# Optimization experiments

Hardware: AMD Instinct MI355X
Metric: run time of the kernel (lower is better)

Reference implementation:

```python
import jax, jax.numpy as jnp
import numpy as np

N, E, DIN, H = 100000, 1600000, 128, 128


def gcn_conv(x, W, b, row, col, ew, n):
    """PyG GCNConv with add_self_loops=True, symmetric normalization.

    deg[i] = sum of edge weights into i (col) + 1 (self loop weight).
    norm_e = deg^{-1/2}[row_e] * ew_e * deg^{-1/2}[col_e]
    out[col] += norm_e * (x @ W)[row]; self-loop contributes deg^{-1}[i] * xw[i].
    """
    xw = x @ W  # [n, H]
    deg = jax.ops.segment_sum(ew, col, num_segments=n) + 1.0  # self-loop weight 1
    dinv = jax.lax.rsqrt(deg)  # deg >= 1 so safe
    norm = dinv[row] * ew * dinv[col]  # [E]
    agg = jax.ops.segment_sum(norm[:, None] * xw[row], col, num_segments=n)
    agg = agg + (dinv * dinv)[:, None] * xw  # self loops
    return agg + b


def setup_inputs() -> dict:
    key = jax.random.key(0)
    ks = jax.random.split(key, 9)
    x = jax.random.normal(ks[0], (N, DIN), jnp.float32)
    edge_index = jax.random.randint(ks[1], (2, E), 0, N, dtype=jnp.int64)
    edge_attr = jax.random.uniform(ks[2], (E,), jnp.float32)
    s_in = 1.0 / np.sqrt(DIN)
    s_h = 1.0 / np.sqrt(H)
    W1 = jax.random.normal(ks[3], (DIN, H), jnp.float32) * s_in
    b1 = jnp.zeros((H,), jnp.float32)
    W2 = jax.random.normal(ks[4], (H, H), jnp.float32) * s_h
    b2 = jnp.zeros((H,), jnp.float32)
    W3 = jax.random.normal(ks[5], (H, H), jnp.float32) * s_h
    b3 = jnp.zeros((H,), jnp.float32)
    return {"x": x, "edge_index": edge_index, "edge_attr": edge_attr,
            "W1": W1, "b1": b1, "W2": W2, "b2": b2, "W3": W3, "b3": b3}


def reference(x, edge_index, edge_attr, W1, b1, W2, b2, W3, b3):
    row, col = edge_index[0], edge_index[1]
    n = x.shape[0]
    h = jax.nn.relu(gcn_conv(x, W1, b1, row, col, edge_attr, n))
    h = jax.nn.relu(gcn_conv(h, W2, b2, row, col, edge_attr, n))
    h = jax.nn.relu(gcn_conv(h, W3, b3, row, col, edge_attr, n))
    return h
```

## Files before the change

### kernel.cpp

```cpp
#include <hip/hip_runtime.h>
#include <hip/hip_fp16.h>

#define CAP 64
#define BSH 7
#define BCAP 2560
#define NBMAX 1024

typedef _Float16 half8 __attribute__((ext_vector_type(8)));
typedef float f32x4 __attribute__((ext_vector_type(4)));


__global__ __launch_bounds__(256) void k_init(int* gcur, int nbkt) {
    int i = blockIdx.x * 256 + threadIdx.x;
    if (i < nbkt) gcur[i] = 0;
}

__global__ __launch_bounds__(256) void k_bucket(const int* __restrict__ row,
                                                const int* __restrict__ col,
                                                const float* __restrict__ ew,
                                                int* gcur, int2* sortedE,
                                                int e, int nbkt) {
    __shared__ int lcnt[NBMAX];
    __shared__ int lbase[NBMAX];
    int tid = threadIdx.x;
    for (int b = tid; b < nbkt; b += 256) lcnt[b] = 0;
    __syncthreads();
    int base = blockIdx.x * 2048;
    int bk[8], rk[8], rx[8], rwi[8];
#pragma unroll
    for (int u = 0; u < 8; ++u) {
        int i = base + tid + u * 256;
        bk[u] = -1;
        if (i < e) {
            int c = col[i];
            bk[u] = c >> BSH;
            rx[u] = row[i] | ((c & ((1 << BSH) - 1)) << 17);
            rwi[u] = __float_as_int(ew[i]);
            rk[u] = atomicAdd(&lcnt[bk[u]], 1);
        }
    }
    __syncthreads();
    for (int b = tid; b < nbkt; b += 256) {
        int c = lcnt[b];
        lbase[b] = c ? atomicAdd(&gcur[b], c) : 0;
    }
    __syncthreads();
#pragma unroll
    for (int u = 0; u < 8; ++u) {
        if (bk[u] >= 0) {
            int pos = lbase[bk[u]] + rk[u];
            if (pos < BCAP) sortedE[(long)bk[u] * BCAP + pos] = make_int2(rx[u], rwi[u]);
        }
    }
}

__global__ __launch_bounds__(256) void k_csr(const int2* __restrict__ sortedE,
                                             const int* __restrict__ gcur,
                                             int2* __restrict__ csr,
                                             int* __restrict__ counts,
                                             float* __restrict__ dinv, int n) {
    int bkt = blockIdx.x;
    __shared__ int c128[128];
    __shared__ float s128[128];
    int tid = threadIdx.x;
    if (tid < 128) { c128[tid] = 0; s128[tid] = 0.f; }
    __syncthreads();
    int cnt = gcur[bkt];
    if (cnt > BCAP) cnt = BCAP;
    for (int j = tid; j < cnt; j += 256) {
        int2 rec = sortedE[(long)bkt * BCAP + j];
        int cl = rec.x >> 17;
        int r0 = rec.x & 0x1FFFF;
        float w = __int_as_float(rec.y);
        int r = atomicAdd(&c128[cl], 1);
        if (r < CAP) csr[((long)((bkt << BSH) + cl)) * CAP + r] = make_int2(r0, rec.y);
        atomicAdd(&s128[cl], w);
    }
    __syncthreads();
    if (tid < 128) {
        int node = (bkt << BSH) + tid;
        if (node < n) {
            int c = c128[tid];
            counts[node] = c < CAP ? c : CAP;
            dinv[node] = rsqrtf(s128[tid] + 1.0f);
        }
    }
}

__global__ __launch_bounds__(256) void k_norm(const int* __restrict__ counts,
                                              const float* __restrict__ dinv,
                                              int2* csr, int n) {
    int gw = (blockIdx.x * 256 + threadIdx.x) >> 6;
    int lane = threadIdx.x & 63;
    if (gw >= n) return;
    int cnt = __builtin_amdgcn_readfirstlane(counts[gw]);
    float dc = dinv[gw];
    if (lane < cnt) {
        long idx = (long)gw * CAP + lane;
        int2 ent = csr[idx];
        float w = dinv[ent.x] * __int_as_float(ent.y) * dc;
        csr[idx] = make_int2(ent.x, __float_as_int(w));
    }
}

__global__ __launch_bounds__(256) void k_wt(const float* __restrict__ W1,
                                            const float* __restrict__ W2,
                                            const float* __restrict__ W3,
                                            __half* __restrict__ Wt) {
    int m = blockIdx.x >> 6;
    int kb = (blockIdx.x & 63) << 1;
    const float* W = m == 0 ? W1 : (m == 1 ? W2 : W3);
    __half* T = Wt + (long)m * 16384;
    int k = kb + (threadIdx.x >> 7);
    int nn = threadIdx.x & 127;
    T[nn * 128 + k] = __float2half(W[k * 128 + nn]);
}


__global__ __launch_bounds__(256) void k_gemm(const float* __restrict__ Xf,
                                              const __half* __restrict__ Xh,
                                              const __half* __restrict__ Wt,
                                              __half* __restrict__ Yh, int n) {
    __shared__ __half Wl[128 * 128];
    int tid = threadIdx.x;
    {
        const uint4* src = (const uint4*)Wt;
#pragma unroll
        for (int i = 0; i < 8; ++i) {
            int c = tid + 256 * i;
            int nrow = c >> 4, k8 = c & 15;
            uint4 v = src[c];
            int byte = nrow * 256 + ((k8 * 16) ^ ((nrow & 7) << 4));
            *(uint4*)((char*)Wl + byte) = v;
        }
    }
    __syncthreads();
    int wid = tid >> 6, lane = tid & 63;
    int l16 = lane & 15, lq = lane >> 4;
    long row0 = (long)blockIdx.x * 128 + wid * 32;
    f32x4 acc[2][8] = {};
#pragma unroll
    for (int ks = 0; ks < 4; ++ks) {
        int k0 = ks * 32;
        half8 a[2];
#pragma unroll
        for (int mt = 0; mt < 2; ++mt) {
            long r = row0 + mt * 16 + l16;
            if (r >= n) r = n - 1;
            if (Xf) {
                const float* px = Xf + r * 128 + k0 + lq * 8;
                float4 f0 = *(const float4*)px;
                float4 f1 = *(const float4*)(px + 4);
                half8 h;
                h[0] = (_Float16)f0.x; h[1] = (_Float16)f0.y;
                h[2] = (_Float16)f0.z; h[3] = (_Float16)f0.w;
                h[4] = (_Float16)f1.x; h[5] = (_Float16)f1.y;
                h[6] = (_Float16)f1.z; h[7] = (_Float16)f1.w;
                a[mt] = h;
            } else {
                a[mt] = *(const half8*)(Xh + r * 128 + k0 + lq * 8);
            }
        }
#pragma unroll
        for (int nt = 0; nt < 8; ++nt) {
            int nrow = nt * 16 + l16;
            int byte = nrow * 256 + (((k0 + lq * 8) * 2) ^ ((nrow & 7) << 4));
            half8 b = *(const half8*)((char*)Wl + byte);
            acc[0][nt] = __builtin_amdgcn_mfma_f32_16x16x32_f16(a[0], b, acc[0][nt], 0, 0, 0);
            acc[1][nt] = __builtin_amdgcn_mfma_f32_16x16x32_f16(a[1], b, acc[1][nt], 0, 0, 0);
        }
    }
#pragma unroll
    for (int mt = 0; mt < 2; ++mt) {
#pragma unroll
        for (int r = 0; r < 4; ++r) {
            long rw = row0 + mt * 16 + lq * 4 + r;
            if (rw < n) {
#pragma unroll
                for (int nt = 0; nt < 8; ++nt) {
                    Yh[rw * 128 + nt * 16 + l16] = __float2half(acc[mt][nt][r]);
                }
            }
        }
    }
}

__global__ __launch_bounds__(256) void k_agg(const int2* __restrict__ csr,
                                             const int* __restrict__ counts,
                                             const float* __restrict__ dinv,
                                             const __half* __restrict__ xwh,
                                             const float* __restrict__ bias,
                                             __half* __restrict__ outh,
                                             float* __restrict__ outf, int n) {
    int gw = (blockIdx.x * 256 + threadIdx.x) >> 6;
    int lane = threadIdx.x & 63;
    if (gw >= n) return;
    int cnt = __builtin_amdgcn_readfirstlane(counts[gw]);
    int g = lane >> 4;
    int c16 = lane & 15;
    float di = dinv[gw];
    half8 sv8 = *(const half8*)(xwh + (long)gw * 128 + c16 * 8);
    float4 bv0 = *(const float4*)(bias + c16 * 8);
    float4 bv1 = *(const float4*)(bias + c16 * 8 + 4);
    int2 ent = make_int2(gw, 0);
    if (lane < cnt) ent = csr[(long)gw * CAP + lane];
    float acc[8] = {};
    int mr = (cnt + 15) & ~15;
    for (int j = 0; j < mr; j += 16) {
        half8 hv[4];
        float wv[4];
#pragma unroll
        for (int q = 0; q < 4; ++q) {
            int r = __shfl(ent.x, j + q * 4 + g);
            hv[q] = *(const half8*)(xwh + (long)r * 128 + c16 * 8);
        }
#pragma unroll
        for (int q = 0; q < 4; ++q) wv[q] = __int_as_float(__shfl(ent.y, j + q * 4 + g));
#pragma unroll
        for (int q = 0; q < 4; ++q) {
#pragma unroll
            for (int t = 0; t < 8; ++t) acc[t] = fmaf(wv[q], (float)hv[q][t], acc[t]);
        }
    }
#pragma unroll
    for (int t = 0; t < 8; ++t) {
        acc[t] += __shfl_xor(acc[t], 16);
        acc[t] += __shfl_xor(acc[t], 32);
    }
    float d2 = di * di;
    float o[8];
    o[0] = fmaxf(acc[0] + d2 * (float)sv8[0] + bv0.x, 0.f);
    o[1] = fmaxf(acc[1] + d2 * (float)sv8[1] + bv0.y, 0.f);
    o[2] = fmaxf(acc[2] + d2 * (float)sv8[2] + bv0.z, 0.f);
    o[3] = fmaxf(acc[3] + d2 * (float)sv8[3] + bv0.w, 0.f);
    o[4] = fmaxf(acc[4] + d2 * (float)sv8[4] + bv1.x, 0.f);
    o[5] = fmaxf(acc[5] + d2 * (float)sv8[5] + bv1.y, 0.f);
    o[6] = fmaxf(acc[6] + d2 * (float)sv8[6] + bv1.z, 0.f);
    o[7] = fmaxf(acc[7] + d2 * (float)sv8[7] + bv1.w, 0.f);
    if (g == 0) {
        if (outh) {
            half8 ho;
#pragma unroll
            for (int t = 0; t < 8; ++t) ho[t] = (_Float16)o[t];
            *(half8*)(outh + (long)gw * 128 + c16 * 8) = ho;
        }
        if (outf) {
            float4 f0 = make_float4(o[0], o[1], o[2], o[3]);
            float4 f1 = make_float4(o[4], o[5], o[6], o[7]);
            *(float4*)(outf + (long)gw * 128 + c16 * 8) = f0;
            *(float4*)(outf + (long)gw * 128 + c16 * 8 + 4) = f1;
        }
    }
}


extern "C" void kernel_launch(void* const* d_in, const int* in_sizes, int n_in,
                              void* d_out, int out_size, void* d_ws, size_t ws_size,
                              hipStream_t stream) {
    const float* x  = (const float*)d_in[0];
    const int*   ei = (const int*)d_in[1];
    const float* ew = (const float*)d_in[2];
    const float* W1 = (const float*)d_in[3];
    const float* b1 = (const float*)d_in[4];
    const float* W2 = (const float*)d_in[5];
    const float* b2 = (const float*)d_in[6];
    const float* W3 = (const float*)d_in[7];
    const float* b3 = (const float*)d_in[8];

    const int n = in_sizes[0] / 128;
    const int e = in_sizes[2];
    const int* row = ei;
    const int* col = ei + e;
    const int nbkt = (n + (1 << BSH) - 1) >> BSH;

    char* p = (char*)d_ws;
    auto alloc = [&](size_t bytes) {
        char* q = p;
        p += (bytes + 255) & ~(size_t)255;
        return q;
    };
    int*    gcur    = (int*)alloc((size_t)nbkt * 4);
    int*    counts  = (int*)alloc((size_t)n * 4);
    float*  dinv    = (float*)alloc((size_t)n * 4);
    __half* Wt      = (__half*)alloc((size_t)3 * 16384 * 2);
    int2*   sortedE = (int2*)alloc((size_t)nbkt * BCAP * 8);
    int2*   csr     = (int2*)alloc((size_t)n * CAP * 8);
    __half* xwh     = (__half*)alloc((size_t)n * 128 * 2);
    __half* h       = (__half*)alloc((size_t)n * 128 * 2);
    (void)ws_size; (void)n_in; (void)out_size;

    int gb = (n + 127) / 128;
    int ab = ((size_t)n * 64 + 255) / 256;
    int sb = (e + 2047) / 2048;

    k_init  <<<(nbkt + 255) / 256, 256, 0, stream>>>(gcur, nbkt);
    k_bucket<<<sb, 256, 0, stream>>>(row, col, ew, gcur, sortedE, e, nbkt);
    k_csr   <<<nbkt, 256, 0, stream>>>(sortedE, gcur, csr, counts, dinv, n);
    k_norm  <<<ab, 256, 0, stream>>>(counts, dinv, csr, n);
    k_wt    <<<192, 256, 0, stream>>>(W1, W2, W3, Wt);

    k_gemm<<<gb, 256, 0, stream>>>(x, (const __half*)nullptr, Wt, xwh, n);
    k_agg <<<ab, 256, 0, stream>>>(csr, counts, dinv, xwh, b1, h, (float*)nullptr, n);
    k_gemm<<<gb, 256, 0, stream>>>((const float*)nullptr, h, Wt + 16384, xwh, n);
    k_agg <<<ab, 256, 0, stream>>>(csr, counts, dinv, xwh, b2, h, (float*)nullptr, n);
    k_gemm<<<gb, 256, 0, stream>>>((const float*)nullptr, h, Wt + 32768, xwh, n);
    k_agg <<<ab, 256, 0, stream>>>(csr, counts, dinv, xwh, b3, (__half*)nullptr, (float*)d_out, n);
}
```

Measured before the change: 316.5 us.

## Pack CSR entries into 32-bit ints with fp16 weights and restructure aggregation loop

Each CSR entry now packs a 17-bit source index and an fp16 edge weight into one 32-bit int, halving CSR storage and the bytes read in normalization and aggregation. The aggregation loop now processes 8 edges per step plus a 4-edge tail instead of rounding up to 16, which avoids padded gathers of the node's own row. The init kernel is replaced with a memset. Weights lose precision by being stored as fp16.

```diff
diff --git a/kernel.cpp b/kernel.cpp
--- a/kernel.cpp
+++ b/kernel.cpp
@@ -9,11 +9,13 @@
 typedef _Float16 half8 __attribute__((ext_vector_type(8)));
 typedef float f32x4 __attribute__((ext_vector_type(4)));
 
-
-__global__ __launch_bounds__(256) void k_init(int* gcur, int nbkt) {
-    int i = blockIdx.x * 256 + threadIdx.x;
-    if (i < nbkt) gcur[i] = 0;
-}
+__device__ __forceinline__ int pack_ent(int r, float w) {
+    return r | ((int)__half_as_ushort(__float2half(w)) << 17);
+}
+__device__ __forceinline__ float ent_w(int ent) {
+    return __half2float(__ushort_as_half((unsigned short)((unsigned)ent >> 17)));
+}
+
 
 __global__ __launch_bounds__(256) void k_bucket(const int* __restrict__ row,
                                                 const int* __restrict__ col,
@@ -56,7 +58,7 @@
 
 __global__ __launch_bounds__(256) void k_csr(const int2* __restrict__ sortedE,
                                              const int* __restrict__ gcur,
-                                             int2* __restrict__ csr,
+                                             int* __restrict__ pcsr,
                                              int* __restrict__ counts,
                                              float* __restrict__ dinv, int n) {
     int bkt = blockIdx.x;
@@ -73,7 +75,7 @@
         int r0 = rec.x & 0x1FFFF;
         float w = __int_as_float(rec.y);
         int r = atomicAdd(&c128[cl], 1);
-        if (r < CAP) csr[((long)((bkt << BSH) + cl)) * CAP + r] = make_int2(r0, rec.y);
+        if (r < CAP) pcsr[((long)((bkt << BSH) + cl)) * CAP + r] = pack_ent(r0, w);
         atomicAdd(&s128[cl], w);
     }
     __syncthreads();
@@ -89,7 +91,7 @@
 
 __global__ __launch_bounds__(256) void k_norm(const int* __restrict__ counts,
                                               const float* __restrict__ dinv,
-                                              int2* csr, int n) {
+                                              int* pcsr, int n) {
     int gw = (blockIdx.x * 256 + threadIdx.x) >> 6;
     int lane = threadIdx.x & 63;
     if (gw >= n) return;
@@ -97,9 +99,10 @@
     float dc = dinv[gw];
     if (lane < cnt) {
         long idx = (long)gw * CAP + lane;
-        int2 ent = csr[idx];
-        float w = dinv[ent.x] * __int_as_float(ent.y) * dc;
-        csr[idx] = make_int2(ent.x, __float_as_int(w));
+        int ent = pcsr[idx];
+        int r = ent & 0x1FFFF;
+        float w = dinv[r] * ent_w(ent) * dc;
+        pcsr[idx] = pack_ent(r, w);
     }
 }
 
@@ -185,7 +188,7 @@
     }
 }
 
-__global__ __launch_bounds__(256) void k_agg(const int2* __restrict__ csr,
+__global__ __launch_bounds__(256) void k_agg(const int* __restrict__ pcsr,
                                              const int* __restrict__ counts,
                                              const float* __restrict__ dinv,
                                              const __half* __restrict__ xwh,
@@ -202,25 +205,30 @@
     half8 sv8 = *(const half8*)(xwh + (long)gw * 128 + c16 * 8);
     float4 bv0 = *(const float4*)(bias + c16 * 8);
     float4 bv1 = *(const float4*)(bias + c16 * 8 + 4);
-    int2 ent = make_int2(gw, 0);
-    if (lane < cnt) ent = csr[(long)gw * CAP + lane];
+    int ent = gw;
+    if (lane < cnt) ent = pcsr[(long)gw * CAP + lane];
     float acc[8] = {};
-    int mr = (cnt + 15) & ~15;
-    for (int j = 0; j < mr; j += 16) {
-        half8 hv[4];
-        float wv[4];
-#pragma unroll
-        for (int q = 0; q < 4; ++q) {
-            int r = __shfl(ent.x, j + q * 4 + g);
-            hv[q] = *(const half8*)(xwh + (long)r * 128 + c16 * 8);
-        }
-#pragma unroll
-        for (int q = 0; q < 4; ++q) wv[q] = __int_as_float(__shfl(ent.y, j + q * 4 + g));
-#pragma unroll
-        for (int q = 0; q < 4; ++q) {
-#pragma unroll
-            for (int t = 0; t < 8; ++t) acc[t] = fmaf(wv[q], (float)hv[q][t], acc[t]);
-        }
+    int j = 0;
+    int mr8 = cnt & ~7;
+    for (; j < mr8; j += 8) {
+        int eA = __shfl(ent, j + g);
+        int eB = __shfl(ent, j + 4 + g);
+        long rA = eA & 0x1FFFF, rB = eB & 0x1FFFF;
+        half8 hA = *(const half8*)(xwh + rA * 128 + c16 * 8);
+        half8 hB = *(const half8*)(xwh + rB * 128 + c16 * 8);
+        float wA = ent_w(eA), wB = ent_w(eB);
+#pragma unroll
+        for (int t = 0; t < 8; ++t) acc[t] = fmaf(wA, (float)hA[t], acc[t]);
+#pragma unroll
+        for (int t = 0; t < 8; ++t) acc[t] = fmaf(wB, (float)hB[t], acc[t]);
+    }
+    for (; j < cnt; j += 4) {
+        int eA = __shfl(ent, j + g);
+        long rA = eA & 0x1FFFF;
+        half8 hA = *(const half8*)(xwh + rA * 128 + c16 * 8);
+        float wA = ent_w(eA);
+#pragma unroll
+        for (int t = 0; t < 8; ++t) acc[t] = fmaf(wA, (float)hA[t], acc[t]);
     }
 #pragma unroll
     for (int t = 0; t < 8; ++t) {
@@ -284,7 +292,7 @@
     float*  dinv    = (float*)alloc((size_t)n * 4);
     __half* Wt      = (__half*)alloc((size_t)3 * 16384 * 2);
     int2*   sortedE = (int2*)alloc((size_t)nbkt * BCAP * 8);
-    int2*   csr     = (int2*)alloc((size_t)n * CAP * 8);
+    int*    pcsr    = (int*)alloc((size_t)n * CAP * 4);
     __half* xwh     = (__half*)alloc((size_t)n * 128 * 2);
     __half* h       = (__half*)alloc((size_t)n * 128 * 2);
     (void)ws_size; (void)n_in; (void)out_size;
@@ -293,16 +301,16 @@
     int ab = ((size_t)n * 64 + 255) / 256;
     int sb = (e + 2047) / 2048;
 
-    k_init  <<<(nbkt + 255) / 256, 256, 0, stream>>>(gcur, nbkt);
+    hipMemsetAsync(gcur, 0, (size_t)nbkt * 4, stream);
     k_bucket<<<sb, 256, 0, stream>>>(row, col, ew, gcur, sortedE, e, nbkt);
-    k_csr   <<<nbkt, 256, 0, stream>>>(sortedE, gcur, csr, counts, dinv, n);
-    k_norm  <<<ab, 256, 0, stream>>>(counts, dinv, csr, n);
+    k_csr   <<<nbkt, 256, 0, stream>>>(sortedE, gcur, pcsr, counts, dinv, n);
+    k_norm  <<<ab, 256, 0, stream>>>(counts, dinv, pcsr, n);
     k_wt    <<<192, 256, 0, stream>>>(W1, W2, W3, Wt);
 
     k_gemm<<<gb, 256, 0, stream>>>(x, (const __half*)nullptr, Wt, xwh, n);
-    k_agg <<<ab, 256, 0, stream>>>(csr, counts, dinv, xwh, b1, h, (float*)nullptr, n);
+    k_agg <<<ab, 256, 0, stream>>>(pcsr, counts, dinv, xwh, b1, h, (float*)nullptr, n);
     k_gemm<<<gb, 256, 0, stream>>>((const float*)nullptr, h, Wt + 16384, xwh, n);
-    k_agg <<<ab, 256, 0, stream>>>(csr, counts, dinv, xwh, b2, h, (float*)nullptr, n);
+    k_agg <<<ab, 256, 0, stream>>>(pcsr, counts, dinv, xwh, b2, h, (float*)nullptr, n);
     k_gemm<<<gb, 256, 0, stream>>>((const float*)nullptr, h, Wt + 32768, xwh, n);
-    k_agg <<<ab, 256, 0, stream>>>(csr, counts, dinv, xwh, b3, (__half*)nullptr, (float*)d_out, n);
-}
+    k_agg <<<ab, 256, 0, stream>>>(pcsr, counts, dinv, xwh, b3, (__half*)nullptr, (float*)d_out, n);
+}
```

Result: no change. 313.3 us (-1.0%).
